# Kernel optimization log

Measured on AMD Instinct MI355X. Metric: run time of the kernel, lower is better.

Reference implementation:

```python
import jax, jax.numpy as jnp
import numpy as np

V, E, H, B, T = 50257, 1024, 1024, 64, 512  # vocab, embed, hidden, batch, steps
PADDING_TOKEN = 0


def setup_inputs() -> dict:
    key = jax.random.key(0)
    ks = jax.random.split(key, 6)
    s = 0.02
    emb = jax.random.normal(ks[0], (V, E), jnp.float32) * s
    emb = emb.at[PADDING_TOKEN].set(0.0)  # padding_idx row is zero
    W_ih = jax.random.normal(ks[1], (4 * H, E), jnp.float32) * s   # torch LSTMCell weight_ih
    W_hh = jax.random.normal(ks[2], (4 * H, H), jnp.float32) * s   # torch LSTMCell weight_hh
    W_cls = jax.random.normal(ks[3], (V, H), jnp.float32) * s      # classifier weight [out,in]
    b_cls = jnp.zeros((V,), jnp.float32)                            # classifier bias
    batch_reviews = jax.random.randint(ks[4], (B, T), 0, V)
    return dict(batch_reviews=batch_reviews, emb=emb, W_ih=W_ih, W_hh=W_hh,
                W_cls=W_cls, b_cls=b_cls)


def _lstm_scan(x_tbe, W_ih, W_hh):
    # torch.nn.LSTMCell math (bias=False); gate order: i, f, g, o
    Bn = x_tbe.shape[1]
    Hn = W_hh.shape[1]

    def cell(carry, x_be):
        h, c = carry
        gates = x_be @ W_ih.T + h @ W_hh.T              # [B, 4H]
        i, f, g, o = jnp.split(gates, 4, axis=-1)
        c2 = jax.nn.sigmoid(f) * c + jax.nn.sigmoid(i) * jnp.tanh(g)
        h2 = jax.nn.sigmoid(o) * jnp.tanh(c2)
        return (h2, c2), None

    init = (jnp.zeros((Bn, Hn), x_tbe.dtype), jnp.zeros((Bn, Hn), x_tbe.dtype))
    (h, c), _ = jax.lax.scan(cell, init, x_tbe)
    return h, c


def reference(batch_reviews, emb, W_ih, W_hh, W_cls, b_cls):
    x = emb[batch_reviews]               # [B, T, E] embedding lookup
    x_tbe = jnp.transpose(x, (1, 0, 2))  # [T, B, E] for time-major scan
    h, c = _lstm_scan(x_tbe, W_ih, W_hh) # final (h, c) state only
    logits = h @ W_cls.T + b_cls         # [B, V]
    return logits, h, c
```

## Files before the change

### kernel.cpp

```cpp
#include <hip/hip_runtime.h>

#define Bn 64
#define Tn 512
#define En 1024
#define Hn 1024
#define Vn 50257
#define CHUNK 64
#define NCHUNK (Tn / CHUNK)
#define AGENT __HIP_MEMORY_SCOPE_AGENT

typedef __attribute__((ext_vector_type(8))) short short8;
typedef __attribute__((ext_vector_type(4))) float f32x4;
typedef __attribute__((ext_vector_type(4))) unsigned int u32x4;
typedef unsigned long long u64;

__device__ __forceinline__ unsigned short f2bf(float f) {
    union { float f; unsigned u; } x; x.f = f;
    unsigned r = x.u + 0x7FFFu + ((x.u >> 16) & 1u);
    return (unsigned short)(r >> 16);
}
__device__ __forceinline__ float sigm(float x) { return 1.0f / (1.0f + __expf(-x)); }
__device__ __forceinline__ float tanh_fast(float x) {
    float e = __expf(2.0f * x);
    return (e - 1.0f) / (e + 1.0f);
}

#define LDH(dst, base, IMM)                                                  \
    asm volatile("global_load_dwordx4 %0, %1, off offset:" #IMM " sc0 sc1"   \
                 : "=v"(dst) : "v"(base) : "memory")

#define VMW(N) do { asm volatile("s_waitcnt vmcnt(" #N ")" ::: "memory");    \
                    __builtin_amdgcn_sched_barrier(0); } while (0)

#define ISSUE_GRP(buf, O0, O1, O2, O3)                                       \
    do {                                                                     \
        LDH((buf)[0], ap0, O0); LDH((buf)[1], ap0, O1);                      \
        LDH((buf)[2], ap0, O2); LDH((buf)[3], ap0, O3);                      \
        LDH((buf)[4], ap1, O0); LDH((buf)[5], ap1, O1);                      \
        LDH((buf)[6], ap1, O2); LDH((buf)[7], ap1, O3);                      \
    } while (0)

#define MFMA_GRP(buf, jb)                                                    \
    do {                                                                     \
        _Pragma("unroll")                                                    \
        for (int jj = 0; jj < 4; ++jj) {                                     \
            union { u32x4 u; short8 s; } f0, f1;                             \
            f0.u = (buf)[jj]; f1.u = (buf)[4 + jj];                          \
            acc[0][0] = __builtin_amdgcn_mfma_f32_16x16x32_bf16(f0.s, breg[0][(jb) + jj], acc[0][0], 0, 0, 0); \
            acc[0][1] = __builtin_amdgcn_mfma_f32_16x16x32_bf16(f0.s, breg[1][(jb) + jj], acc[0][1], 0, 0, 0); \
            acc[1][0] = __builtin_amdgcn_mfma_f32_16x16x32_bf16(f1.s, breg[0][(jb) + jj], acc[1][0], 0, 0, 0); \
            acc[1][1] = __builtin_amdgcn_mfma_f32_16x16x32_bf16(f1.s, breg[1][(jb) + jj], acc[1][1], 0, 0, 0); \
        }                                                                    \
    } while (0)

__global__ __launch_bounds__(256)
void cvt_f32_bf16(const float* __restrict__ src, unsigned short* __restrict__ dst, int n4) {
    int i = blockIdx.x * 256 + threadIdx.x;
    if (i < n4) {
        float4 v = reinterpret_cast<const float4*>(src)[i];
        ushort4 o;
        o.x = f2bf(v.x); o.y = f2bf(v.y); o.z = f2bf(v.z); o.w = f2bf(v.w);
        reinterpret_cast<ushort4*>(dst)[i] = o;
    }
}

__global__ __launch_bounds__(256)
void gather_x(const int* __restrict__ tokens, const float* __restrict__ emb,
              unsigned short* __restrict__ X, int t0) {
    const int r = blockIdx.x;
    const int trel = r >> 6, b = r & 63;
    const int tok = tokens[b * Tn + t0 + trel];
    const float* src = emb + (size_t)tok * En;
    const int k = threadIdx.x * 4;
    float4 v = *reinterpret_cast<const float4*>(src + k);
    ushort4 o;
    o.x = f2bf(v.x); o.y = f2bf(v.y); o.z = f2bf(v.z); o.w = f2bf(v.w);
    *reinterpret_cast<ushort4*>(X + (size_t)r * En + k) = o;
}

__global__ __launch_bounds__(256)
void gemm_gin(const unsigned short* __restrict__ X, const unsigned short* __restrict__ Wih,
              float* __restrict__ G) {
    __shared__ __align__(16) unsigned short As[128][72];
    __shared__ __align__(16) unsigned short Bs[128][72];

    const int tid = threadIdx.x;
    const int bx = blockIdx.x & 31;
    const int by = blockIdx.x >> 5;
    const int w = tid >> 6, l = tid & 63;
    const int wr = w >> 1, wc = w & 1;

    f32x4 acc[4][4];
#pragma unroll
    for (int i = 0; i < 4; ++i)
#pragma unroll
        for (int j = 0; j < 4; ++j) acc[i][j] = (f32x4){0.f, 0.f, 0.f, 0.f};

    const int koff = (l >> 4) * 8;

    for (int kk = 0; kk < En / 64; ++kk) {
        __syncthreads();
#pragma unroll
        for (int j = 0; j < 4; ++j) {
            const int u = tid * 4 + j;
            const int row = u >> 3, ku = (u & 7) * 8;
            *reinterpret_cast<short8*>(&As[row][ku]) =
                *reinterpret_cast<const short8*>(X + (size_t)(by * 128 + row) * En + kk * 64 + ku);
            *reinterpret_cast<short8*>(&Bs[row][ku]) =
                *reinterpret_cast<const short8*>(Wih + (size_t)(bx * 128 + row) * En + kk * 64 + ku);
        }
        __syncthreads();

#pragma unroll
        for (int kc = 0; kc < 2; ++kc) {
            const int k0 = kc * 32 + koff;
            short8 af[4], bf[4];
#pragma unroll
            for (int i = 0; i < 4; ++i)
                af[i] = *reinterpret_cast<const short8*>(&As[wr * 64 + i * 16 + (l & 15)][k0]);
#pragma unroll
            for (int j = 0; j < 4; ++j)
                bf[j] = *reinterpret_cast<const short8*>(&Bs[wc * 64 + j * 16 + (l & 15)][k0]);
#pragma unroll
            for (int i = 0; i < 4; ++i)
#pragma unroll
                for (int j = 0; j < 4; ++j)
                    acc[i][j] = __builtin_amdgcn_mfma_f32_16x16x32_bf16(af[i], bf[j], acc[i][j], 0, 0, 0);
        }
    }

    const int rr = 4 * (l >> 4);
#pragma unroll
    for (int i = 0; i < 4; ++i) {
        const int row = by * 128 + wr * 64 + i * 16 + rr;
#pragma unroll
        for (int j = 0; j < 4; ++j) {
            const int col = bx * 128 + wc * 64 + j * 16 + (l & 15);
#pragma unroll
            for (int r = 0; r < 4; ++r)
                G[(size_t)(row + r) * 4096 + col] = acc[i][j][r];
        }
    }
}

__global__ __launch_bounds__(256, 1)
void lstm_chunk(const float* __restrict__ G, const unsigned short* __restrict__ Whh,
                unsigned short* __restrict__ h0, unsigned short* __restrict__ h1,
                float* __restrict__ c_state, unsigned* __restrict__ flags, int t0,
                float* __restrict__ out_h, float* __restrict__ out_c)
{
    __shared__ __align__(16) float red[2][2][2][64][4];

    const int tid = threadIdx.x;
    const int b = blockIdx.x;
    const int w = tid >> 6, l = tid & 63;
    const int kh = w & 1, rh = w >> 1;
    const int koff = (l >> 4) * 8;
    const int lc = l & 15;
    const int hcol = b * 8 + (l & 7);

    short8 breg[2][16];
#pragma unroll
    for (int ct = 0; ct < 2; ++ct) {
        const int gate = ct * 2 + (lc >> 3);
        const unsigned short* wrow = Whh + ((size_t)gate * Hn + (b * 8 + (lc & 7))) * Hn;
#pragma unroll
        for (int j = 0; j < 16; ++j)
            breg[ct][j] = *reinterpret_cast<const short8*>(wrow + (kh * 16 + j) * 32 + koff);
    }

    float c_reg[2][4];
    if (kh == 0) {
#pragma unroll
        for (int rt = 0; rt < 2; ++rt)
#pragma unroll
            for (int r = 0; r < 4; ++r)
                c_reg[rt][r] = c_state[(rh * 32 + rt * 16 + ((l >> 4) << 2) + r) * Hn + hcol];
    }

    const int sg = lc >> 3;
    const int gc0 = sg * Hn + hcol;
    const int gc1 = (2 + sg) * Hn + hcol;

    for (int s = 0; s < CHUNK; ++s) {
        const int t = t0 + s;
        const unsigned short* hin = (t & 1) ? h1 : h0;
        unsigned short* hout = (t & 1) ? h0 : h1;

        float g0[2][4], g1[2][4];
        if (kh == 0) {
            const float* Gt = G + (size_t)s * Bn * 4096;
#pragma unroll
            for (int rt = 0; rt < 2; ++rt) {
                const int rowbase = rh * 32 + rt * 16 + ((l >> 4) << 2);
#pragma unroll
                for (int r = 0; r < 4; ++r) {
                    g0[rt][r] = Gt[(size_t)(rowbase + r) * 4096 + gc0];
                    g1[rt][r] = Gt[(size_t)(rowbase + r) * 4096 + gc1];
                }
            }
        }

        const unsigned short* ap0 =
            hin + (size_t)(rh * 32 + (l & 15)) * Hn + kh * 512 + koff;
        const unsigned short* ap1 =
            hin + (size_t)(rh * 32 + 16 + (l & 15)) * Hn + kh * 512 + koff;

        f32x4 acc[2][2];
        acc[0][0] = acc[0][1] = acc[1][0] = acc[1][1] = (f32x4){0.f, 0.f, 0.f, 0.f};

        u32x4 bufA[8], bufB[8], bufC[8], bufD[8];
        ISSUE_GRP(bufA, 0,   64,  128, 192);
        ISSUE_GRP(bufB, 256, 320, 384, 448);
        ISSUE_GRP(bufC, 512, 576, 640, 704);
        ISSUE_GRP(bufD, 768, 832, 896, 960);

        VMW(24); MFMA_GRP(bufA, 0);
        VMW(16); MFMA_GRP(bufB, 4);
        VMW(8);  MFMA_GRP(bufC, 8);
        VMW(0);  MFMA_GRP(bufD, 12);

        if (kh == 1) {
#pragma unroll
            for (int rt = 0; rt < 2; ++rt)
#pragma unroll
                for (int ct = 0; ct < 2; ++ct)
                    *reinterpret_cast<f32x4*>(&red[rh][rt][ct][l][0]) = acc[rt][ct];
        }
        __syncthreads();

        if (kh == 0) {
#pragma unroll
            for (int rt = 0; rt < 2; ++rt) {
                const int rowbase = rh * 32 + rt * 16 + ((l >> 4) << 2);
                f32x4 a0 = acc[rt][0] + *reinterpret_cast<f32x4*>(&red[rh][rt][0][l][0]);
                f32x4 a1 = acc[rt][1] + *reinterpret_cast<f32x4*>(&red[rh][rt][1][l][0]);
#pragma unroll
                for (int r = 0; r < 4; ++r) {
                    float v0 = a0[r] + g0[rt][r];
                    float v1 = a1[r] + g1[rt][r];
                    float p0 = __shfl_xor(v0, 8);
                    float p1 = __shfl_xor(v1, 8);
                    float iv = (l & 8) ? p0 : v0;
                    float fv = (l & 8) ? v0 : p0;
                    float gv = (l & 8) ? p1 : v1;
                    float ov = (l & 8) ? v1 : p1;
                    float cn = sigm(fv) * c_reg[rt][r] + sigm(iv) * tanh_fast(gv);
                    float hn = sigm(ov) * tanh_fast(cn);
                    c_reg[rt][r] = cn;
                    unsigned hb = f2bf(hn);
                    unsigned partner = (unsigned)__shfl_xor((int)hb, 1);
                    if (!(l & 8) && !(l & 1)) {
                        unsigned val = (hb & 0xFFFFu) | (partner << 16);
                        __hip_atomic_store(
                            (unsigned*)(hout + (size_t)(rowbase + r) * Hn + hcol),
                            val, __ATOMIC_RELAXED, AGENT);
                    }
                    if (t == Tn - 1 && !(l & 8)) {
                        out_h[(rowbase + r) * Hn + hcol] = hn;
                        out_c[(rowbase + r) * Hn + hcol] = cn;
                    }
                }
            }
        }

        asm volatile("s_waitcnt vmcnt(0)" ::: "memory");
        __syncthreads();
        if (tid == 0)
            __hip_atomic_store(&flags[b * 32], (unsigned)(t + 1), __ATOMIC_RELAXED, AGENT);
        if (tid < 128) {
            const unsigned target = (unsigned)(t + 1);
            int guard = 0;
            while (__hip_atomic_load(&flags[tid * 32], __ATOMIC_RELAXED, AGENT) < target &&
                   guard < (1 << 16)) {
                __builtin_amdgcn_s_sleep(1);
                ++guard;
            }
        }
        __syncthreads();
    }

    if (kh == 0 && !(l & 8)) {
#pragma unroll
        for (int rt = 0; rt < 2; ++rt)
#pragma unroll
            for (int r = 0; r < 4; ++r)
                c_state[(rh * 32 + rt * 16 + ((l >> 4) << 2) + r) * Hn + hcol] = c_reg[rt][r];
    }
}

__global__ __launch_bounds__(256)
void classifier(const unsigned short* __restrict__ h,
                const float* __restrict__ Wcls, const float* __restrict__ bcls,
                float* __restrict__ logits)
{
    __shared__ __align__(16) unsigned short Al[64][72];
    __shared__ __align__(16) unsigned short Bl[64][72];

    const int tid = threadIdx.x;
    const int v0 = blockIdx.x * 64;
    const int w = tid >> 6, l = tid & 63;
    const int lrow = tid >> 2, q = tid & 3;
    const int v = v0 + lrow;

    const unsigned short* hrow = h + lrow * Hn;
    const float* wrow = Wcls + (size_t)v * Hn;

    f32x4 acc[4];
#pragma unroll
    for (int ct = 0; ct < 4; ++ct) acc[ct] = (f32x4){0.f, 0.f, 0.f, 0.f};

    const int arow = w * 16 + (l & 15);
    const int koff = (l >> 4) * 8;

    for (int ch = 0; ch < 16; ++ch) {
        const int k0 = ch * 64;
        __syncthreads();
#pragma unroll
        for (int i2 = 0; i2 < 4; ++i2) {
            const int k = q * 4 + i2 * 16;
            *reinterpret_cast<ushort4*>(&Al[lrow][k]) =
                *reinterpret_cast<const ushort4*>(hrow + k0 + k);
            if (v < Vn) {
                float4 x = *reinterpret_cast<const float4*>(wrow + k0 + k);
                Bl[lrow][k + 0] = f2bf(x.x); Bl[lrow][k + 1] = f2bf(x.y);
                Bl[lrow][k + 2] = f2bf(x.z); Bl[lrow][k + 3] = f2bf(x.w);
            } else {
                ushort4 z; z.x = z.y = z.z = z.w = 0;
                *reinterpret_cast<ushort4*>(&Bl[lrow][k]) = z;
            }
        }
        __syncthreads();

        short8 a0 = *reinterpret_cast<const short8*>(&Al[arow][koff]);
        short8 a1 = *reinterpret_cast<const short8*>(&Al[arow][32 + koff]);
#pragma unroll
        for (int ct = 0; ct < 4; ++ct) {
            const int bcol = ct * 16 + (l & 15);
            short8 b0 = *reinterpret_cast<const short8*>(&Bl[bcol][koff]);
            short8 b1 = *reinterpret_cast<const short8*>(&Bl[bcol][32 + koff]);
            acc[ct] = __builtin_amdgcn_mfma_f32_16x16x32_bf16(a0, b0, acc[ct], 0, 0, 0);
            acc[ct] = __builtin_amdgcn_mfma_f32_16x16x32_bf16(a1, b1, acc[ct], 0, 0, 0);
        }
    }

    const int rr0 = w * 16 + (l >> 4) * 4;
#pragma unroll
    for (int ct = 0; ct < 4; ++ct) {
        const int vv = v0 + ct * 16 + (l & 15);
        if (vv < Vn) {
            float bb = bcls[vv];
#pragma unroll
            for (int r = 0; r < 4; ++r)
                logits[(size_t)(rr0 + r) * Vn + vv] = acc[ct][r] + bb;
        }
    }
}

extern "C" void kernel_launch(void* const* d_in, const int* in_sizes, int n_in,
                              void* d_out, int out_size, void* d_ws, size_t ws_size,
                              hipStream_t stream)
{
    const int*   tokens = (const int*)d_in[0];
    const float* emb    = (const float*)d_in[1];
    const float* W_ih   = (const float*)d_in[2];
    const float* W_hh   = (const float*)d_in[3];
    const float* W_cls  = (const float*)d_in[4];
    const float* b_cls  = (const float*)d_in[5];
    float* out = (float*)d_out;

    char* ws = (char*)d_ws;
    unsigned short* hbuf0 = (unsigned short*)ws;
    unsigned short* hbuf1 = (unsigned short*)(ws + 131072);
    float*          cst   = (float*)(ws + 262144);
    unsigned*       flags = (unsigned*)(ws + 524288);
    unsigned short* Wih_b = (unsigned short*)(ws + 540672);
    unsigned short* Whh_b = (unsigned short*)(ws + 540672 + 8388608);
    unsigned short* Xb    = (unsigned short*)(ws + 540672 + 2 * 8388608);
    float*          Gb    = (float*)(ws + 540672 + 3 * 8388608);

    hipMemsetAsync(ws, 0, 540672, stream);

    const int n4 = (4 * Hn * En) / 4;
    cvt_f32_bf16<<<n4 / 256, 256, 0, stream>>>(W_ih, Wih_b, n4);
    cvt_f32_bf16<<<n4 / 256, 256, 0, stream>>>(W_hh, Whh_b, n4);

    float* out_h = out + (size_t)Bn * Vn;
    float* out_c = out_h + Bn * Hn;

    for (int c = 0; c < NCHUNK; ++c) {
        int t0 = c * CHUNK;
        gather_x<<<CHUNK * Bn, 256, 0, stream>>>(tokens, emb, Xb, t0);
        gemm_gin<<<32 * 32, 256, 0, stream>>>(Xb, Wih_b, Gb);
        lstm_chunk<<<128, 256, 0, stream>>>(Gb, Whh_b, hbuf0, hbuf1,
                                            cst, flags, t0, out_h, out_c);
    }

    classifier<<<(Vn + 63) / 64, 256, 0, stream>>>(hbuf0, W_cls, b_cls, out);
}
```

Measured before the change: 4.610 ms.

## Overlap next-chunk input GEMM with LSTM recurrence in fused kernel, bf16 gate buffer

The LSTM chunk kernel now launches 256 blocks. 128 run the recurrence, and the other 128 compute the input-projection GEMM for the next chunk into a double-buffered gate buffer, so serial GEMM launches no longer sit on the critical path. The precomputed gates are stored in bf16 instead of fp32, halving that traffic. The gate values for the next step are prefetched while the block waits at the inter-block barrier. The risks are that the GEMM blocks compete for CUs and memory bandwidth with the latency-bound recurrence, and that 256 co-resident blocks must fit for the spin barrier to avoid deadlock. bf16 gates also add rounding error.

```diff
diff --git a/kernel.cpp b/kernel.cpp
--- a/kernel.cpp
+++ b/kernel.cpp
@@ -12,13 +12,15 @@
 typedef __attribute__((ext_vector_type(8))) short short8;
 typedef __attribute__((ext_vector_type(4))) float f32x4;
 typedef __attribute__((ext_vector_type(4))) unsigned int u32x4;
-typedef unsigned long long u64;
 
 __device__ __forceinline__ unsigned short f2bf(float f) {
     union { float f; unsigned u; } x; x.f = f;
     unsigned r = x.u + 0x7FFFu + ((x.u >> 16) & 1u);
     return (unsigned short)(r >> 16);
 }
+__device__ __forceinline__ float bf2f(unsigned short u) {
+    union { unsigned u; float f; } x; x.u = ((unsigned)u) << 16; return x.f;
+}
 __device__ __forceinline__ float sigm(float x) { return 1.0f / (1.0f + __expf(-x)); }
 __device__ __forceinline__ float tanh_fast(float x) {
     float e = __expf(2.0f * x);
@@ -28,10 +30,8 @@
 #define LDH(dst, base, IMM)                                                  \
     asm volatile("global_load_dwordx4 %0, %1, off offset:" #IMM " sc0 sc1"   \
                  : "=v"(dst) : "v"(base) : "memory")
-
 #define VMW(N) do { asm volatile("s_waitcnt vmcnt(" #N ")" ::: "memory");    \
                     __builtin_amdgcn_sched_barrier(0); } while (0)
-
 #define ISSUE_GRP(buf, O0, O1, O2, O3)                                       \
     do {                                                                     \
         LDH((buf)[0], ap0, O0); LDH((buf)[1], ap0, O1);                      \
@@ -39,7 +39,6 @@
         LDH((buf)[4], ap1, O0); LDH((buf)[5], ap1, O1);                      \
         LDH((buf)[6], ap1, O2); LDH((buf)[7], ap1, O3);                      \
     } while (0)
-
 #define MFMA_GRP(buf, jb)                                                    \
     do {                                                                     \
         _Pragma("unroll")                                                    \
@@ -78,25 +77,20 @@
     *reinterpret_cast<ushort4*>(X + (size_t)r * En + k) = o;
 }
 
-__global__ __launch_bounds__(256)
-void gemm_gin(const unsigned short* __restrict__ X, const unsigned short* __restrict__ Wih,
-              float* __restrict__ G) {
-    __shared__ __align__(16) unsigned short As[128][72];
-    __shared__ __align__(16) unsigned short Bs[128][72];
-
-    const int tid = threadIdx.x;
-    const int bx = blockIdx.x & 31;
-    const int by = blockIdx.x >> 5;
+__device__ __forceinline__ void gemm_tile(
+    const unsigned short* __restrict__ X, const unsigned short* __restrict__ Wih,
+    unsigned short* __restrict__ G, int bx, int by,
+    unsigned short (*As)[72], unsigned short (*Bs)[72], int tid)
+{
     const int w = tid >> 6, l = tid & 63;
     const int wr = w >> 1, wc = w & 1;
+    const int koff = (l >> 4) * 8;
 
     f32x4 acc[4][4];
 #pragma unroll
     for (int i = 0; i < 4; ++i)
 #pragma unroll
         for (int j = 0; j < 4; ++j) acc[i][j] = (f32x4){0.f, 0.f, 0.f, 0.f};
-
-    const int koff = (l >> 4) * 8;
 
     for (int kk = 0; kk < En / 64; ++kk) {
         __syncthreads();
@@ -138,20 +132,46 @@
             const int col = bx * 128 + wc * 64 + j * 16 + (l & 15);
 #pragma unroll
             for (int r = 0; r < 4; ++r)
-                G[(size_t)(row + r) * 4096 + col] = acc[i][j][r];
-        }
-    }
+                G[(size_t)(row + r) * 4096 + col] = f2bf(acc[i][j][r]);
+        }
+    }
+}
+
+__global__ __launch_bounds__(256)
+void gemm_gin(const unsigned short* __restrict__ X, const unsigned short* __restrict__ Wih,
+              unsigned short* __restrict__ G) {
+    __shared__ __align__(16) unsigned short As[128][72];
+    __shared__ __align__(16) unsigned short Bs[128][72];
+    gemm_tile(X, Wih, G, blockIdx.x & 31, blockIdx.x >> 5, As, Bs, threadIdx.x);
 }
 
 __global__ __launch_bounds__(256, 1)
-void lstm_chunk(const float* __restrict__ G, const unsigned short* __restrict__ Whh,
+void lstm_fused(const unsigned short* __restrict__ Gcur, unsigned short* __restrict__ Gnext,
+                const unsigned short* __restrict__ Xnext, const unsigned short* __restrict__ Wih,
+                const unsigned short* __restrict__ Whh,
                 unsigned short* __restrict__ h0, unsigned short* __restrict__ h1,
-                float* __restrict__ c_state, unsigned* __restrict__ flags, int t0,
+                float* __restrict__ c_state, unsigned* __restrict__ flags, int t0, int do_gemm,
                 float* __restrict__ out_h, float* __restrict__ out_c)
 {
-    __shared__ __align__(16) float red[2][2][2][64][4];
+    __shared__ __align__(16) char smem[2 * 128 * 72 * 2];
 
     const int tid = threadIdx.x;
+
+    if (blockIdx.x >= 128) {
+        if (!do_gemm) return;
+        unsigned short (*As)[72] = reinterpret_cast<unsigned short(*)[72]>(smem);
+        unsigned short (*Bs)[72] = reinterpret_cast<unsigned short(*)[72]>(smem + 128 * 72 * 2);
+        const int base = (blockIdx.x - 128) * 8;
+        for (int tt = 0; tt < 8; ++tt) {
+            const int tile = base + tt;
+            gemm_tile(Xnext, Wih, Gnext, tile & 31, tile >> 5, As, Bs, tid);
+        }
+        return;
+    }
+
+    typedef float RedT[2][2][64][4];
+    RedT* red = reinterpret_cast<RedT*>(smem);
+
     const int b = blockIdx.x;
     const int w = tid >> 6, l = tid & 63;
     const int kh = w & 1, rh = w >> 1;
@@ -182,24 +202,23 @@
     const int gc0 = sg * Hn + hcol;
     const int gc1 = (2 + sg) * Hn + hcol;
 
+    unsigned short gp0[2][4], gp1[2][4];
+    if (kh == 0) {
+#pragma unroll
+        for (int rt = 0; rt < 2; ++rt) {
+            const int rowbase = rh * 32 + rt * 16 + ((l >> 4) << 2);
+#pragma unroll
+            for (int r = 0; r < 4; ++r) {
+                gp0[rt][r] = Gcur[(size_t)(rowbase + r) * 4096 + gc0];
+                gp1[rt][r] = Gcur[(size_t)(rowbase + r) * 4096 + gc1];
+            }
+        }
+    }
+
     for (int s = 0; s < CHUNK; ++s) {
         const int t = t0 + s;
         const unsigned short* hin = (t & 1) ? h1 : h0;
         unsigned short* hout = (t & 1) ? h0 : h1;
-
-        float g0[2][4], g1[2][4];
-        if (kh == 0) {
-            const float* Gt = G + (size_t)s * Bn * 4096;
-#pragma unroll
-            for (int rt = 0; rt < 2; ++rt) {
-                const int rowbase = rh * 32 + rt * 16 + ((l >> 4) << 2);
-#pragma unroll
-                for (int r = 0; r < 4; ++r) {
-                    g0[rt][r] = Gt[(size_t)(rowbase + r) * 4096 + gc0];
-                    g1[rt][r] = Gt[(size_t)(rowbase + r) * 4096 + gc1];
-                }
-            }
-        }
 
         const unsigned short* ap0 =
             hin + (size_t)(rh * 32 + (l & 15)) * Hn + kh * 512 + koff;
@@ -237,8 +256,8 @@
                 f32x4 a1 = acc[rt][1] + *reinterpret_cast<f32x4*>(&red[rh][rt][1][l][0]);
 #pragma unroll
                 for (int r = 0; r < 4; ++r) {
-                    float v0 = a0[r] + g0[rt][r];
-                    float v1 = a1[r] + g1[rt][r];
+                    float v0 = a0[r] + bf2f(gp0[rt][r]);
+                    float v1 = a1[r] + bf2f(gp1[rt][r]);
                     float p0 = __shfl_xor(v0, 8);
                     float p1 = __shfl_xor(v1, 8);
                     float iv = (l & 8) ? p0 : v0;
@@ -268,10 +287,25 @@
         __syncthreads();
         if (tid == 0)
             __hip_atomic_store(&flags[b * 32], (unsigned)(t + 1), __ATOMIC_RELAXED, AGENT);
-        if (tid < 128) {
+
+        if (kh == 0 && s + 1 < CHUNK) {
+            const unsigned short* Gt = Gcur + (size_t)(s + 1) * Bn * 4096;
+#pragma unroll
+            for (int rt = 0; rt < 2; ++rt) {
+                const int rowbase = rh * 32 + rt * 16 + ((l >> 4) << 2);
+#pragma unroll
+                for (int r = 0; r < 4; ++r) {
+                    gp0[rt][r] = Gt[(size_t)(rowbase + r) * 4096 + gc0];
+                    gp1[rt][r] = Gt[(size_t)(rowbase + r) * 4096 + gc1];
+                }
+            }
+        }
+
+        {
             const unsigned target = (unsigned)(t + 1);
+            const int pf = (tid & 127) * 32;
             int guard = 0;
-            while (__hip_atomic_load(&flags[tid * 32], __ATOMIC_RELAXED, AGENT) < target &&
+            while (__hip_atomic_load(&flags[pf], __ATOMIC_RELAXED, AGENT) < target &&
                    guard < (1 << 16)) {
                 __builtin_amdgcn_s_sleep(1);
                 ++guard;
@@ -377,7 +411,8 @@
     unsigned short* Wih_b = (unsigned short*)(ws + 540672);
     unsigned short* Whh_b = (unsigned short*)(ws + 540672 + 8388608);
     unsigned short* Xb    = (unsigned short*)(ws + 540672 + 2 * 8388608);
-    float*          Gb    = (float*)(ws + 540672 + 3 * 8388608);
+    unsigned short* Gb0   = (unsigned short*)(ws + 540672 + 3 * 8388608);
+    unsigned short* Gb1   = (unsigned short*)(ws + 540672 + 3 * 8388608 + 33554432);
 
     hipMemsetAsync(ws, 0, 540672, stream);
 
@@ -388,12 +423,18 @@
     float* out_h = out + (size_t)Bn * Vn;
     float* out_c = out_h + Bn * Hn;
 
+    gather_x<<<CHUNK * Bn, 256, 0, stream>>>(tokens, emb, Xb, 0);
+    gemm_gin<<<32 * 32, 256, 0, stream>>>(Xb, Wih_b, Gb0);
+
+    unsigned short* Gbuf[2] = {Gb0, Gb1};
     for (int c = 0; c < NCHUNK; ++c) {
-        int t0 = c * CHUNK;
-        gather_x<<<CHUNK * Bn, 256, 0, stream>>>(tokens, emb, Xb, t0);
-        gemm_gin<<<32 * 32, 256, 0, stream>>>(Xb, Wih_b, Gb);
-        lstm_chunk<<<128, 256, 0, stream>>>(Gb, Whh_b, hbuf0, hbuf1,
-                                            cst, flags, t0, out_h, out_c);
+        const int do_gemm = (c + 1 < NCHUNK) ? 1 : 0;
+        if (do_gemm)
+            gather_x<<<CHUNK * Bn, 256, 0, stream>>>(tokens, emb, Xb, (c + 1) * CHUNK);
+        lstm_fused<<<256, 256, 0, stream>>>(Gbuf[c & 1], Gbuf[(c + 1) & 1], Xb,
+                                            Wih_b, Whh_b, hbuf0, hbuf1,
+                                            cst, flags, c * CHUNK, do_gemm,
+                                            out_h, out_c);
     }
 
     classifier<<<(Vn + 63) / 64, 256, 0, stream>>>(hbuf0, W_cls, b_cls, out);
```

New measurement: 4.287 ms. 7.0% less time.
